# Kernel optimization log

Hardware: AMD Instinct MI355X
Metric: run time of the kernel (lower is better)

The kernel has to match this reference:

```python
import jax, jax.numpy as jnp
import numpy as np
from jax import lax

T, B, DIN, H, OUT, L = 256, 128, 20, 1024, 1095, 3


def setup_inputs() -> dict:
    key = jax.random.key(0)
    ks = jax.random.split(key, 8)
    x = jax.random.normal(ks[0], (T, B, DIN), dtype=jnp.float32)
    c = jnp.zeros((L, B, H), dtype=jnp.float32)  # accepted but unused, as in original
    s_in = 1.0 / np.sqrt(DIN)
    s_h = 1.0 / np.sqrt(H)
    W1 = jax.random.uniform(ks[1], (DIN, H), jnp.float32, -s_in, s_in)
    b1 = jnp.zeros((H,), jnp.float32)
    # SRU per-layer weights: W maps h -> [z | f_pre | r_pre] (3H); biases for f and r gates
    W_sru = jax.random.uniform(ks[2], (L, H, 3 * H), jnp.float32, -s_h, s_h)
    bf_sru = jnp.zeros((L, H), jnp.float32)
    br_sru = jnp.zeros((L, H), jnp.float32)
    W3 = jax.random.uniform(ks[3], (H, OUT), jnp.float32, -s_h, s_h)
    b3 = jnp.zeros((OUT,), jnp.float32)
    return {"x": x, "c": c, "W1": W1, "b1": b1, "W_sru": W_sru,
            "bf_sru": bf_sru, "br_sru": br_sru, "W3": W3, "b3": b3}


def _sru_layer(h, W, bf, br):
    """One SRU layer. h: (T,B,H). Returns (h_out (T,B,H), c_final (B,H))."""
    U = jnp.einsum('tbh,hk->tbk', h, W)                    # (T,B,3H) big GEMM up front
    z, f_pre, r_pre = jnp.split(U, 3, axis=-1)
    f = jax.nn.sigmoid(f_pre + bf)
    r = jax.nn.sigmoid(r_pre + br)

    def step(c_prev, inp):
        f_t, z_t, r_t, x_t = inp
        c_t = f_t * c_prev + (1.0 - f_t) * z_t
        h_t = r_t * c_t + (1.0 - r_t) * x_t               # highway (input_size == hidden_size)
        return c_t, h_t

    c0 = jnp.zeros(h.shape[1:], h.dtype)
    c_final, h_out = lax.scan(step, c0, (f, z, r, h))
    return h_out, c_final


def reference(x, c, W1, b1, W_sru, bf_sru, br_sru, W3, b3):
    t, b, _ = x.shape
    h = (x.reshape(t * b, -1) @ W1 + b1).reshape(t, b, H)  # Dense_layer1
    c_finals = []
    for l in range(L):                                      # 3 SRU layers (fixed count)
        h, c_l = _sru_layer(h, W_sru[l], bf_sru[l], br_sru[l])
        c_finals.append(c_l)
    out = h.reshape(t * b, H) @ W3 + b3                     # Dense_layer3 -> (T*B, OUT)
    return out, jnp.stack(c_finals)                         # ((T*B,OUT), (L,B,H))
```

## Files before the change

kernel.cpp:

```cpp
#include <hip/hip_runtime.h>
#include <hip/hip_bf16.h>


#define T_DIM 256
#define B_DIM 128
#define DIN 20
#define H_DIM 1024
#define OUT_DIM 1095
#define L_DIM 3
#define M_DIM (T_DIM * B_DIM)
#define H3 (3 * H_DIM)
#define OUT_ELEMS ((size_t)M_DIM * OUT_DIM)

typedef __bf16 bf16x8 __attribute__((ext_vector_type(8)));
typedef __bf16 bf16x4 __attribute__((ext_vector_type(4)));
typedef __bf16 bf16x2 __attribute__((ext_vector_type(2)));
typedef float f32x4 __attribute__((ext_vector_type(4)));

__device__ __forceinline__ void async16(const __bf16* g, __bf16* l) {
  __builtin_amdgcn_global_load_lds(
      (const __attribute__((address_space(1))) void*)g,
      (__attribute__((address_space(3))) void*)l, 16, 0, 0);
}

__global__ void transpose_sru(const float* __restrict__ W, __bf16* __restrict__ Wt) {
  __shared__ float tile[32][33];
  int l = blockIdx.z;
  int j0 = blockIdx.x * 32;
  int i0 = blockIdx.y * 32;
  int tx = threadIdx.x, ty = threadIdx.y;
  const float* Wl = W + (size_t)l * H_DIM * H3;
  __bf16* Wtl = Wt + (size_t)l * H_DIM * H3;
#pragma unroll
  for (int r = 0; r < 4; r++)
    tile[ty + r * 8][tx] = Wl[(size_t)(i0 + ty + r * 8) * H3 + j0 + tx];
  __syncthreads();
#pragma unroll
  for (int r = 0; r < 4; r++)
    Wtl[(size_t)(j0 + ty + r * 8) * H_DIM + i0 + tx] = (__bf16)tile[tx][ty + r * 8];
}

__global__ void transpose_w3(const float* __restrict__ W, __bf16* __restrict__ Wt) {
  __shared__ float tile[32][33];
  int j0 = blockIdx.x * 32;
  int i0 = blockIdx.y * 32;
  int tx = threadIdx.x, ty = threadIdx.y;
#pragma unroll
  for (int r = 0; r < 4; r++) {
    int j = j0 + tx;
    if (j < OUT_DIM)
      tile[ty + r * 8][tx] = W[(size_t)(i0 + ty + r * 8) * OUT_DIM + j];
  }
  __syncthreads();
#pragma unroll
  for (int r = 0; r < 4; r++) {
    int j = j0 + ty + r * 8;
    if (j < OUT_DIM)
      Wt[(size_t)j * H_DIM + i0 + tx] = (__bf16)tile[tx][ty + r * 8];
  }
}

__global__ __launch_bounds__(256) void dense1(const float* __restrict__ x,
                                              const float* __restrict__ W1,
                                              const float* __restrict__ b1,
                                              __bf16* __restrict__ h) {
  __shared__ float wsl[DIN * 256];
  __shared__ float xs[128 * DIN];
  int tid = threadIdx.x;
  int m0 = blockIdx.x * 128;
  int n0 = blockIdx.y * 256;
#pragma unroll
  for (int k = 0; k < DIN; k++) wsl[k * 256 + tid] = W1[k * H_DIM + n0 + tid];
  for (int idx = tid; idx < 128 * DIN; idx += 256) xs[idx] = x[(size_t)m0 * DIN + idx];
  __syncthreads();
  float wreg[DIN];
#pragma unroll
  for (int k = 0; k < DIN; k++) wreg[k] = wsl[k * 256 + tid];
  float bias = b1[n0 + tid];
  for (int m = 0; m < 128; m++) {
    float acc = bias;
#pragma unroll
    for (int k = 0; k < DIN; k++) acc += xs[m * DIN + k] * wreg[k];
    h[(size_t)(m0 + m) * H_DIM + n0 + tid] = (__bf16)acc;
  }
}


template <int MH>
__device__ __forceinline__ void mfma16(f32x4 (&acc)[8][4], const bf16x8 (&aF)[4],
                                       const bf16x8 (&bF)[4]) {
  __builtin_amdgcn_s_setprio(1);
#pragma unroll
  for (int i = 0; i < 4; ++i)
#pragma unroll
    for (int fn = 0; fn < 4; ++fn)
      acc[MH * 4 + i][fn] =
          __builtin_amdgcn_mfma_f32_16x16x32_bf16(bF[fn], aF[i], acc[MH * 4 + i][fn], 0, 0, 0);
  __builtin_amdgcn_s_setprio(0);
}

__global__ __launch_bounds__(512, 2) void gemm_gate(const __bf16* __restrict__ A,
                                                    const __bf16* __restrict__ Bt,
                                                    __bf16* __restrict__ U,
                                                    const float* __restrict__ biasf,
                                                    const float* __restrict__ biasr) {
  __shared__ __align__(16) char lds[131072];
  int tid = threadIdx.x;
  int lane = tid & 63;
  int w = tid >> 6;
  int wm = w & 1, wn = w >> 1;

  int gx = gridDim.x;
  int lin = blockIdx.y * gx + blockIdx.x;
  int xcd = lin & 7;
  int kk = lin >> 3;
  int bx, by;
  if ((gx >> 3) == 8) { bx = xcd * 8 + (kk & 7); by = kk >> 3; }
  else                { bx = xcd * 4 + (kk & 3); by = kk >> 2; }
  int m0 = bx * 256, n0 = by * 256;

  int r8row = w * 8 + (lane >> 3);
  int cse = (((lane & 7) ^ (lane >> 3)) * 8);
  int l15 = lane & 15;
  int quad = lane >> 4;
  int asw = (lane & 7) << 4;

  f32x4 acc[8][4];
#pragma unroll
  for (int i = 0; i < 8; ++i)
#pragma unroll
    for (int j = 0; j < 4; ++j) acc[i][j] = (f32x4)0.f;
  bf16x8 aF[4], bF[4];

#define STAGE_TILE(T_) do { int _t = (T_); int _b = (_t & 1) * 65536;            \
    _Pragma("unroll") for (int _u = 0; _u < 4; ++_u)                             \
      async16(A + (size_t)(m0 + _u * 64 + r8row) * 1024 + _t * 64 + cse,         \
              (__bf16*)(lds + _b + _u * 8192 + w * 1024));                       \
    _Pragma("unroll") for (int _u = 0; _u < 4; ++_u)                             \
      async16(Bt + (size_t)(n0 + _u * 64 + r8row) * 1024 + _t * 64 + cse,        \
              (__bf16*)(lds + _b + 32768 + _u * 8192 + w * 1024)); } while (0)

#define LOAD_A(MH_, KS_) do {                                                    \
    _Pragma("unroll") for (int i = 0; i < 4; ++i)                                \
      aF[i] = *(const bf16x8*)(lds + bufc +                                      \
                (wm * 128 + (MH_) * 64 + i * 16 + l15) * 128 +                   \
                ((quad * 16 + (KS_) * 64) ^ asw)); } while (0)

#define LOAD_B(KS_) do {                                                         \
    _Pragma("unroll") for (int i = 0; i < 4; ++i)                                \
      bF[i] = *(const bf16x8*)(lds + bufc + 32768 +                              \
                (wn * 64 + i * 16 + l15) * 128 +                                 \
                ((quad * 16 + (KS_) * 64) ^ asw)); } while (0)

  STAGE_TILE(0);
  __syncthreads();

#pragma unroll 2
  for (int t = 0; t < 16; ++t) {
    int bufc = (t & 1) * 65536;
    if (t < 15) STAGE_TILE(t + 1);
    LOAD_B(0);
    LOAD_A(0, 0); mfma16<0>(acc, aF, bF);
    LOAD_A(1, 0); mfma16<1>(acc, aF, bF);
    LOAD_B(1);
    LOAD_A(0, 1); mfma16<0>(acc, aF, bF);
    LOAD_A(1, 1); mfma16<1>(acc, aF, bF);
    __syncthreads();
  }
#undef STAGE_TILE
#undef LOAD_A
#undef LOAD_B

  int gN[4];
  f32x4 bV[4];
#pragma unroll
  for (int fn = 0; fn < 4; ++fn) {
    int gc = n0 + wn * 64 + fn * 16 + quad * 4;
    int g = gc >> 10;
    gN[fn] = g;
    if (g == 1) bV[fn] = *(const f32x4*)&biasf[gc - 1024];
    else if (g == 2) bV[fn] = *(const f32x4*)&biasr[gc - 2048];
    else bV[fn] = (f32x4)0.f;
  }
#pragma unroll
  for (int fm = 0; fm < 8; ++fm) {
    int m = wm * 128 + fm * 16 + l15;
    char* rowp = lds + m * 512;
    int msw = (m & 7) << 4;
#pragma unroll
    for (int fn = 0; fn < 4; ++fn) {
      int nq = wn * 64 + fn * 16 + quad * 4;
      f32x4 v = acc[fm][fn];
      if (gN[fn] != 0) {
#pragma unroll
        for (int j = 0; j < 4; ++j) v[j] = 1.f / (1.f + __expf(-(v[j] + bV[fn][j])));
      }
      bf16x4 o;
#pragma unroll
      for (int j = 0; j < 4; ++j) o[j] = (__bf16)v[j];
      *(bf16x4*)(rowp + ((nq * 2) ^ msw)) = o;
    }
  }
  __syncthreads();
#pragma unroll
  for (int it = 0; it < 16; ++it) {
    int idx = it * 512 + tid;
    int row = idx >> 5;
    int ce = (idx & 31) * 8;
    bf16x8 val = *(const bf16x8*)(lds + row * 512 + ((ce * 2) ^ ((row & 7) << 4)));
    *(bf16x8*)&U[(size_t)(m0 + row) * H3 + n0 + ce] = val;
  }
}

__global__ __launch_bounds__(256) void gemm_out(const __bf16* __restrict__ A,
                                                const __bf16* __restrict__ Bt,
                                                float* __restrict__ C,
                                                const float* __restrict__ bias0) {
  constexpr int K = 1024;
  __shared__ __align__(16) __bf16 sA[128 * 32];
  __shared__ __align__(16) __bf16 sB[128 * 32];
  int tid = threadIdx.x;
  int lane = tid & 63;
  int wave = tid >> 6;
  int wm = wave & 1, wn = wave >> 1;
  int m0 = blockIdx.x * 128;
  int n0 = blockIdx.y * 128;

  f32x4 acc[4][4];
#pragma unroll
  for (int i = 0; i < 4; i++)
#pragma unroll
    for (int j = 0; j < 4; j++) acc[i][j] = (f32x4)0.f;

  int lrow = lane >> 2;
  int lcol8 = (lane & 3) * 8;
  int q8 = (lane >> 4) * 8;
  int l15 = lane & 15;

  for (int k0 = 0; k0 < K; k0 += 32) {
    __syncthreads();
#pragma unroll
    for (int i = 0; i < 2; i++) {
      int j = wave * 2 + i;
      int arow = m0 + j * 16 + lrow;
      async16(A + (size_t)arow * K + k0 + lcol8, &sA[j * 512]);
      int brow = n0 + j * 16 + lrow;
      brow = brow < OUT_DIM - 1 ? brow : OUT_DIM - 1;
      async16(Bt + (size_t)brow * K + k0 + lcol8, &sB[j * 512]);
    }
    __syncthreads();
    bf16x8 aF[4], bF[4];
#pragma unroll
    for (int i = 0; i < 4; i++) {
      aF[i] = *(const bf16x8*)&sA[(wm * 64 + i * 16 + l15) * 32 + q8];
      bF[i] = *(const bf16x8*)&sB[(wn * 64 + i * 16 + l15) * 32 + q8];
    }
#pragma unroll
    for (int mi = 0; mi < 4; mi++)
#pragma unroll
      for (int ni = 0; ni < 4; ni++)
        acc[mi][ni] = __builtin_amdgcn_mfma_f32_16x16x32_bf16(aF[mi], bF[ni], acc[mi][ni], 0, 0, 0);
  }

  int quad = lane >> 4;
#pragma unroll
  for (int mi = 0; mi < 4; mi++) {
    int rowBase = m0 + wm * 64 + mi * 16 + quad * 4;
#pragma unroll
    for (int ni = 0; ni < 4; ni++) {
      int col = n0 + wn * 64 + ni * 16 + l15;
      if (col < OUT_DIM) {
        float badd = bias0[col];
#pragma unroll
        for (int r = 0; r < 4; r++)
          C[(size_t)(rowBase + r) * OUT_DIM + col] = acc[mi][ni][r] + badd;
      }
    }
  }
}

__global__ __launch_bounds__(256) void sru_scan(const __bf16* __restrict__ U,
                                                __bf16* __restrict__ h,
                                                float* __restrict__ cst,
                                                float* __restrict__ cfin,
                                                int tc, int first, int last) {
  int id = blockIdx.x * 256 + threadIdx.x;
  int n2 = id * 2;
  int b = n2 >> 10;
  int hh = n2 & 1023;
  float c0, c1;
  if (first) { c0 = 0.f; c1 = 0.f; }
  else { c0 = cst[n2]; c1 = cst[n2 + 1]; }
  size_t ub = (size_t)b * H3 + hh;
  size_t xb = (size_t)b * H_DIM + hh;
  const size_t strideU = (size_t)B_DIM * H3;
  const size_t strideH = (size_t)B_DIM * H_DIM;
  for (int t = 0; t < tc; t++) {
    bf16x2 z2 = *(const bf16x2*)&U[ub];
    bf16x2 f2 = *(const bf16x2*)&U[ub + 1024];
    bf16x2 r2 = *(const bf16x2*)&U[ub + 2048];
    bf16x2 x2 = *(const bf16x2*)&h[xb];
    float f0 = (float)f2[0], f1 = (float)f2[1];
    float r0 = (float)r2[0], r1 = (float)r2[1];
    c0 = f0 * c0 + (1.f - f0) * (float)z2[0];
    c1 = f1 * c1 + (1.f - f1) * (float)z2[1];
    float h0 = r0 * c0 + (1.f - r0) * (float)x2[0];
    float h1 = r1 * c1 + (1.f - r1) * (float)x2[1];
    bf16x2 o;
    o[0] = (__bf16)h0;
    o[1] = (__bf16)h1;
    *(bf16x2*)&h[xb] = o;
    ub += strideU;
    xb += strideH;
  }
  cst[n2] = c0;
  cst[n2 + 1] = c1;
  if (last) {
    cfin[n2] = c0;
    cfin[n2 + 1] = c1;
  }
}

extern "C" void kernel_launch(void* const* d_in, const int* in_sizes, int n_in,
                              void* d_out, int out_size, void* d_ws, size_t ws_size,
                              hipStream_t stream) {
  const float* x = (const float*)d_in[0];
  const float* W1 = (const float*)d_in[2];
  const float* b1 = (const float*)d_in[3];
  const float* Wsru = (const float*)d_in[4];
  const float* bf_s = (const float*)d_in[5];
  const float* br_s = (const float*)d_in[6];
  const float* W3 = (const float*)d_in[7];
  const float* b3 = (const float*)d_in[8];
  float* out = (float*)d_out;

  const size_t kFixed = 67108864ull + 18874368ull + 2242560ull + 524288ull;
  int tch = (ws_size >= kFixed + (size_t)128 * B_DIM * H3 * 2) ? 128 : 64;
  int mch = tch * B_DIM;
  int nch = T_DIM / tch;

  char* wsb = (char*)d_ws;
  __bf16* h = (__bf16*)(wsb);
  __bf16* U = (__bf16*)(wsb + 67108864);
  char* wAfter = wsb + 67108864 + (size_t)mch * H3 * 2;
  __bf16* Wt = (__bf16*)(wAfter);
  __bf16* W3t = (__bf16*)(wAfter + 18874368);
  float* cst = (float*)(wAfter + 18874368 + 2242560);

  transpose_sru<<<dim3(H3 / 32, H_DIM / 32, L_DIM), dim3(32, 8), 0, stream>>>(Wsru, Wt);
  transpose_w3<<<dim3((OUT_DIM + 31) / 32, H_DIM / 32), dim3(32, 8), 0, stream>>>(W3, W3t);
  dense1<<<dim3(M_DIM / 128, H_DIM / 256), 256, 0, stream>>>(x, W1, b1, h);

  for (int l = 0; l < L_DIM; l++) {
    const __bf16* Wtl = Wt + (size_t)l * H_DIM * H3;
    const float* bfl = bf_s + l * H_DIM;
    const float* brl = br_s + l * H_DIM;
    float* cfin = out + OUT_ELEMS + (size_t)l * B_DIM * H_DIM;
    for (int ch = 0; ch < nch; ch++) {
      __bf16* hA = h + (size_t)ch * mch * H_DIM;
      gemm_gate<<<dim3(mch / 256, H3 / 256), 512, 0, stream>>>(hA, Wtl, U, bfl, brl);
      sru_scan<<<dim3(B_DIM * H_DIM / 512), 256, 0, stream>>>(
          U, hA, cst, cfin, tch, ch == 0 ? 1 : 0, ch == (nch - 1) ? 1 : 0);
    }
  }

  gemm_out<<<dim3(M_DIM / 128, (OUT_DIM + 127) / 128), 256, 0, stream>>>(h, W3t, out, b3);
}
```

Measured before the change: 1.248 ms.

## Reuse tuned 256x256 double-buffered GEMM for output layer and prefetch scan inputs

The final dense layer now runs on the same 256x256-tile, 512-thread, LDS double-buffered GEMM used for the SRU gate projection, replacing the simpler 128x128 single-stage kernel. The kernel is templated on an epilogue mode, and in output mode it clamps B rows so the ragged N edge stays in bounds. The SRU scan also software-pipelines its loads, fetching step t+1's U and h values while computing step t, to hide memory latency on the serial recurrence. Risks include wasted work on the padded last N tile (1095 spread over 5 tiles) and a generalized swizzle that assumes the grid width divided by 8 is a power of two.

```diff
diff --git a/kernel.cpp b/kernel.cpp
--- a/kernel.cpp
+++ b/kernel.cpp
@@ -86,24 +86,31 @@
 }
 
 
-template <int MH>
+template <int MH, int EPI>
 __device__ __forceinline__ void mfma16(f32x4 (&acc)[8][4], const bf16x8 (&aF)[4],
                                        const bf16x8 (&bF)[4]) {
   __builtin_amdgcn_s_setprio(1);
 #pragma unroll
   for (int i = 0; i < 4; ++i)
 #pragma unroll
-    for (int fn = 0; fn < 4; ++fn)
-      acc[MH * 4 + i][fn] =
-          __builtin_amdgcn_mfma_f32_16x16x32_bf16(bF[fn], aF[i], acc[MH * 4 + i][fn], 0, 0, 0);
+    for (int fn = 0; fn < 4; ++fn) {
+      if (EPI == 1)
+        acc[MH * 4 + i][fn] =
+            __builtin_amdgcn_mfma_f32_16x16x32_bf16(bF[fn], aF[i], acc[MH * 4 + i][fn], 0, 0, 0);
+      else
+        acc[MH * 4 + i][fn] =
+            __builtin_amdgcn_mfma_f32_16x16x32_bf16(aF[i], bF[fn], acc[MH * 4 + i][fn], 0, 0, 0);
+    }
   __builtin_amdgcn_s_setprio(0);
 }
 
-__global__ __launch_bounds__(512, 2) void gemm_gate(const __bf16* __restrict__ A,
-                                                    const __bf16* __restrict__ Bt,
-                                                    __bf16* __restrict__ U,
-                                                    const float* __restrict__ biasf,
-                                                    const float* __restrict__ biasr) {
+template <int EPI>
+__global__ __launch_bounds__(512, 2) void gemm256(const __bf16* __restrict__ A,
+                                                  const __bf16* __restrict__ Bt,
+                                                  void* __restrict__ Cv,
+                                                  const float* __restrict__ bias0,
+                                                  const float* __restrict__ bias1,
+                                                  int Ntotal, int ldc) {
   __shared__ __align__(16) char lds[131072];
   int tid = threadIdx.x;
   int lane = tid & 63;
@@ -114,9 +121,10 @@
   int lin = blockIdx.y * gx + blockIdx.x;
   int xcd = lin & 7;
   int kk = lin >> 3;
-  int bx, by;
-  if ((gx >> 3) == 8) { bx = xcd * 8 + (kk & 7); by = kk >> 3; }
-  else                { bx = xcd * 4 + (kk & 3); by = kk >> 2; }
+  int bpx = gx >> 3;
+  int sh = __builtin_ctz(bpx);
+  int bx = xcd * bpx + (kk & (bpx - 1));
+  int by = kk >> sh;
   int m0 = bx * 256, n0 = by * 256;
 
   int r8row = w * 8 + (lane >> 3);
@@ -136,9 +144,12 @@
     _Pragma("unroll") for (int _u = 0; _u < 4; ++_u)                             \
       async16(A + (size_t)(m0 + _u * 64 + r8row) * 1024 + _t * 64 + cse,         \
               (__bf16*)(lds + _b + _u * 8192 + w * 1024));                       \
-    _Pragma("unroll") for (int _u = 0; _u < 4; ++_u)                             \
-      async16(Bt + (size_t)(n0 + _u * 64 + r8row) * 1024 + _t * 64 + cse,        \
-              (__bf16*)(lds + _b + 32768 + _u * 8192 + w * 1024)); } while (0)
+    _Pragma("unroll") for (int _u = 0; _u < 4; ++_u) {                           \
+      int _br = n0 + _u * 64 + r8row;                                            \
+      if (EPI == 0 && _br > Ntotal - 1) _br = Ntotal - 1;                        \
+      async16(Bt + (size_t)_br * 1024 + _t * 64 + cse,                           \
+              (__bf16*)(lds + _b + 32768 + _u * 8192 + w * 1024));               \
+    } } while (0)
 
 #define LOAD_A(MH_, KS_) do {                                                    \
     _Pragma("unroll") for (int i = 0; i < 4; ++i)                                \
@@ -160,120 +171,72 @@
     int bufc = (t & 1) * 65536;
     if (t < 15) STAGE_TILE(t + 1);
     LOAD_B(0);
-    LOAD_A(0, 0); mfma16<0>(acc, aF, bF);
-    LOAD_A(1, 0); mfma16<1>(acc, aF, bF);
+    LOAD_A(0, 0); mfma16<0, EPI>(acc, aF, bF);
+    LOAD_A(1, 0); mfma16<1, EPI>(acc, aF, bF);
     LOAD_B(1);
-    LOAD_A(0, 1); mfma16<0>(acc, aF, bF);
-    LOAD_A(1, 1); mfma16<1>(acc, aF, bF);
+    LOAD_A(0, 1); mfma16<0, EPI>(acc, aF, bF);
+    LOAD_A(1, 1); mfma16<1, EPI>(acc, aF, bF);
     __syncthreads();
   }
 #undef STAGE_TILE
 #undef LOAD_A
 #undef LOAD_B
 
-  int gN[4];
-  f32x4 bV[4];
-#pragma unroll
-  for (int fn = 0; fn < 4; ++fn) {
-    int gc = n0 + wn * 64 + fn * 16 + quad * 4;
-    int g = gc >> 10;
-    gN[fn] = g;
-    if (g == 1) bV[fn] = *(const f32x4*)&biasf[gc - 1024];
-    else if (g == 2) bV[fn] = *(const f32x4*)&biasr[gc - 2048];
-    else bV[fn] = (f32x4)0.f;
-  }
-#pragma unroll
-  for (int fm = 0; fm < 8; ++fm) {
-    int m = wm * 128 + fm * 16 + l15;
-    char* rowp = lds + m * 512;
-    int msw = (m & 7) << 4;
+  if (EPI == 1) {
+    __bf16* U = (__bf16*)Cv;
+    int gN[4];
+    f32x4 bV[4];
 #pragma unroll
     for (int fn = 0; fn < 4; ++fn) {
-      int nq = wn * 64 + fn * 16 + quad * 4;
-      f32x4 v = acc[fm][fn];
-      if (gN[fn] != 0) {
-#pragma unroll
-        for (int j = 0; j < 4; ++j) v[j] = 1.f / (1.f + __expf(-(v[j] + bV[fn][j])));
+      int gc = n0 + wn * 64 + fn * 16 + quad * 4;
+      int g = gc >> 10;
+      gN[fn] = g;
+      if (g == 1) bV[fn] = *(const f32x4*)&bias0[gc - 1024];
+      else if (g == 2) bV[fn] = *(const f32x4*)&bias1[gc - 2048];
+      else bV[fn] = (f32x4)0.f;
+    }
+#pragma unroll
+    for (int fm = 0; fm < 8; ++fm) {
+      int m = wm * 128 + fm * 16 + l15;
+      char* rowp = lds + m * 512;
+      int msw = (m & 7) << 4;
+#pragma unroll
+      for (int fn = 0; fn < 4; ++fn) {
+        int nq = wn * 64 + fn * 16 + quad * 4;
+        f32x4 v = acc[fm][fn];
+        if (gN[fn] != 0) {
+#pragma unroll
+          for (int j = 0; j < 4; ++j) v[j] = 1.f / (1.f + __expf(-(v[j] + bV[fn][j])));
+        }
+        bf16x4 o;
+#pragma unroll
+        for (int j = 0; j < 4; ++j) o[j] = (__bf16)v[j];
+        *(bf16x4*)(rowp + ((nq * 2) ^ msw)) = o;
       }
-      bf16x4 o;
-#pragma unroll
-      for (int j = 0; j < 4; ++j) o[j] = (__bf16)v[j];
-      *(bf16x4*)(rowp + ((nq * 2) ^ msw)) = o;
-    }
-  }
-  __syncthreads();
-#pragma unroll
-  for (int it = 0; it < 16; ++it) {
-    int idx = it * 512 + tid;
-    int row = idx >> 5;
-    int ce = (idx & 31) * 8;
-    bf16x8 val = *(const bf16x8*)(lds + row * 512 + ((ce * 2) ^ ((row & 7) << 4)));
-    *(bf16x8*)&U[(size_t)(m0 + row) * H3 + n0 + ce] = val;
-  }
-}
-
-__global__ __launch_bounds__(256) void gemm_out(const __bf16* __restrict__ A,
-                                                const __bf16* __restrict__ Bt,
-                                                float* __restrict__ C,
-                                                const float* __restrict__ bias0) {
-  constexpr int K = 1024;
-  __shared__ __align__(16) __bf16 sA[128 * 32];
-  __shared__ __align__(16) __bf16 sB[128 * 32];
-  int tid = threadIdx.x;
-  int lane = tid & 63;
-  int wave = tid >> 6;
-  int wm = wave & 1, wn = wave >> 1;
-  int m0 = blockIdx.x * 128;
-  int n0 = blockIdx.y * 128;
-
-  f32x4 acc[4][4];
-#pragma unroll
-  for (int i = 0; i < 4; i++)
-#pragma unroll
-    for (int j = 0; j < 4; j++) acc[i][j] = (f32x4)0.f;
-
-  int lrow = lane >> 2;
-  int lcol8 = (lane & 3) * 8;
-  int q8 = (lane >> 4) * 8;
-  int l15 = lane & 15;
-
-  for (int k0 = 0; k0 < K; k0 += 32) {
+    }
     __syncthreads();
 #pragma unroll
-    for (int i = 0; i < 2; i++) {
-      int j = wave * 2 + i;
-      int arow = m0 + j * 16 + lrow;
-      async16(A + (size_t)arow * K + k0 + lcol8, &sA[j * 512]);
-      int brow = n0 + j * 16 + lrow;
-      brow = brow < OUT_DIM - 1 ? brow : OUT_DIM - 1;
-      async16(Bt + (size_t)brow * K + k0 + lcol8, &sB[j * 512]);
-    }
-    __syncthreads();
-    bf16x8 aF[4], bF[4];
-#pragma unroll
-    for (int i = 0; i < 4; i++) {
-      aF[i] = *(const bf16x8*)&sA[(wm * 64 + i * 16 + l15) * 32 + q8];
-      bF[i] = *(const bf16x8*)&sB[(wn * 64 + i * 16 + l15) * 32 + q8];
-    }
-#pragma unroll
-    for (int mi = 0; mi < 4; mi++)
-#pragma unroll
-      for (int ni = 0; ni < 4; ni++)
-        acc[mi][ni] = __builtin_amdgcn_mfma_f32_16x16x32_bf16(aF[mi], bF[ni], acc[mi][ni], 0, 0, 0);
-  }
-
-  int quad = lane >> 4;
-#pragma unroll
-  for (int mi = 0; mi < 4; mi++) {
-    int rowBase = m0 + wm * 64 + mi * 16 + quad * 4;
-#pragma unroll
-    for (int ni = 0; ni < 4; ni++) {
-      int col = n0 + wn * 64 + ni * 16 + l15;
-      if (col < OUT_DIM) {
-        float badd = bias0[col];
-#pragma unroll
-        for (int r = 0; r < 4; r++)
-          C[(size_t)(rowBase + r) * OUT_DIM + col] = acc[mi][ni][r] + badd;
+    for (int it = 0; it < 16; ++it) {
+      int idx = it * 512 + tid;
+      int row = idx >> 5;
+      int ce = (idx & 31) * 8;
+      bf16x8 val = *(const bf16x8*)(lds + row * 512 + ((ce * 2) ^ ((row & 7) << 4)));
+      *(bf16x8*)&U[(size_t)(m0 + row) * ldc + n0 + ce] = val;
+    }
+  } else {
+    float* C = (float*)Cv;
+#pragma unroll
+    for (int fm = 0; fm < 8; ++fm) {
+      int rowBase = m0 + wm * 128 + fm * 16 + quad * 4;
+#pragma unroll
+      for (int fn = 0; fn < 4; ++fn) {
+        int col = n0 + wn * 64 + fn * 16 + l15;
+        if (col < Ntotal) {
+          float badd = bias0[col];
+#pragma unroll
+          for (int r = 0; r < 4; ++r)
+            C[(size_t)(rowBase + r) * ldc + col] = acc[fm][fn][r] + badd;
+        }
       }
     }
   }
@@ -295,11 +258,19 @@
   size_t xb = (size_t)b * H_DIM + hh;
   const size_t strideU = (size_t)B_DIM * H3;
   const size_t strideH = (size_t)B_DIM * H_DIM;
-  for (int t = 0; t < tc; t++) {
-    bf16x2 z2 = *(const bf16x2*)&U[ub];
-    bf16x2 f2 = *(const bf16x2*)&U[ub + 1024];
-    bf16x2 r2 = *(const bf16x2*)&U[ub + 2048];
-    bf16x2 x2 = *(const bf16x2*)&h[xb];
+
+  bf16x2 z2 = *(const bf16x2*)&U[ub];
+  bf16x2 f2 = *(const bf16x2*)&U[ub + 1024];
+  bf16x2 r2 = *(const bf16x2*)&U[ub + 2048];
+  bf16x2 x2 = *(const bf16x2*)&h[xb];
+
+  for (int t = 0; t < tc - 1; t++) {
+    size_t ubn = ub + strideU, xbn = xb + strideH;
+    bf16x2 z2n = *(const bf16x2*)&U[ubn];
+    bf16x2 f2n = *(const bf16x2*)&U[ubn + 1024];
+    bf16x2 r2n = *(const bf16x2*)&U[ubn + 2048];
+    bf16x2 x2n = *(const bf16x2*)&h[xbn];
+
     float f0 = (float)f2[0], f1 = (float)f2[1];
     float r0 = (float)r2[0], r1 = (float)r2[1];
     c0 = f0 * c0 + (1.f - f0) * (float)z2[0];
@@ -310,8 +281,21 @@
     o[0] = (__bf16)h0;
     o[1] = (__bf16)h1;
     *(bf16x2*)&h[xb] = o;
-    ub += strideU;
-    xb += strideH;
+
+    z2 = z2n; f2 = f2n; r2 = r2n; x2 = x2n;
+    ub = ubn; xb = xbn;
+  }
+  {
+    float f0 = (float)f2[0], f1 = (float)f2[1];
+    float r0 = (float)r2[0], r1 = (float)r2[1];
+    c0 = f0 * c0 + (1.f - f0) * (float)z2[0];
+    c1 = f1 * c1 + (1.f - f1) * (float)z2[1];
+    float h0 = r0 * c0 + (1.f - r0) * (float)x2[0];
+    float h1 = r1 * c1 + (1.f - r1) * (float)x2[1];
+    bf16x2 o;
+    o[0] = (__bf16)h0;
+    o[1] = (__bf16)h1;
+    *(bf16x2*)&h[xb] = o;
   }
   cst[n2] = c0;
   cst[n2 + 1] = c1;
@@ -358,11 +342,12 @@
     float* cfin = out + OUT_ELEMS + (size_t)l * B_DIM * H_DIM;
     for (int ch = 0; ch < nch; ch++) {
       __bf16* hA = h + (size_t)ch * mch * H_DIM;
-      gemm_gate<<<dim3(mch / 256, H3 / 256), 512, 0, stream>>>(hA, Wtl, U, bfl, brl);
+      gemm256<1><<<dim3(mch / 256, H3 / 256), 512, 0, stream>>>(hA, Wtl, U, bfl, brl, H3, H3);
       sru_scan<<<dim3(B_DIM * H_DIM / 512), 256, 0, stream>>>(
           U, hA, cst, cfin, tch, ch == 0 ? 1 : 0, ch == (nch - 1) ? 1 : 0);
     }
   }
 
-  gemm_out<<<dim3(M_DIM / 128, (OUT_DIM + 127) / 128), 256, 0, stream>>>(h, W3t, out, b3);
-}
+  gemm256<0><<<dim3(M_DIM / 256, (OUT_DIM + 255) / 256), 512, 0, stream>>>(
+      h, W3t, out, b3, nullptr, OUT_DIM, OUT_DIM);
+}
```

After: 1.239 ms. Within noise of the previous version (-0.7%).
